# Kernel tuning notes

Hardware: AMD Instinct MI355X
Metric: run time of the kernel (lower is better)

Reference implementation:

```python
import jax, jax.numpy as jnp
import numpy as np

M, K, D_M = 8, 256, 128
N, D = 65536, M * D_M


def setup_inputs() -> dict:
    key = jax.random.key(0)
    kx, kc = jax.random.split(key)
    x = jax.random.normal(kx, (N, D), dtype=jnp.float32)
    codebook = jax.random.normal(kc, (M, K, D_M), dtype=jnp.float32)
    return {"x": x, "codebook": codebook, "temperature": 1}


def _distance(x, codebook):
    # x: (n, d) -> (n, m, d_m); codebook: (m, k, d_m)
    n = x.shape[0]
    m, k, d_m = codebook.shape
    xr = x.reshape(n, m, d_m)
    x2 = jnp.sum(xr * xr, axis=-1, keepdims=True)        # (n, m, 1)
    c2 = jnp.sum(codebook * codebook, axis=-1)            # (m, k)
    inter = jnp.einsum('nmd,mkd->nmk', xr, codebook)      # (n, m, k)
    return x2 + c2 - 2.0 * inter                          # (n, m, k)


def reference(x, codebook, temperature):
    # Soft-PQ (trainable path): soft assignment over codewords per subspace,
    # then reconstruct from the codebook.
    n = x.shape[0]
    m, k, d_m = codebook.shape
    distance = _distance(x, codebook)                     # (n, m, k)
    soft = jax.nn.softmax(-distance / jnp.float32(temperature), axis=-1)
    quantized = jnp.einsum('nmk,mkd->nmd', soft, codebook).reshape(n, m * d_m)
    return quantized
```

## Files before the change

### kernel.cpp

```cpp
#include <hip/hip_runtime.h>

#define LOG2E 1.4426950408889634f

typedef _Float16 half8 __attribute__((ext_vector_type(8)));
typedef float floatx16 __attribute__((ext_vector_type(16)));

__device__ __forceinline__ void g2l16(const void* g, void* l) {
  __builtin_amdgcn_global_load_lds(
      (__attribute__((address_space(1))) void*)(unsigned long long)(g),
      (__attribute__((address_space(3))) void*)(unsigned int)(unsigned long long)(l),
      16, 0, 0);
}

__global__ __launch_bounds__(128, 4) void prep_kernel(
    const float* __restrict__ cb, const int* __restrict__ tptr,
    _Float16* __restrict__ cb16, _Float16* __restrict__ cbT,
    float* __restrict__ c2s) {
  int mk = blockIdx.x;
  int m = mk >> 8, k = mk & 255;
  int d = threadIdx.x;
  float v = cb[(size_t)mk * 128 + d];
  _Float16 h = (_Float16)v;
  cb16[(size_t)mk * 128 + d] = h;
  int kp = ((k & 31) << 3) | (k >> 5);
  cbT[((size_t)m * 128 + d) * 256 + kp] = h;
  float sq = v * v;
#pragma unroll
  for (int o = 0; o < 6; ++o) sq += __shfl_xor(sq, 1 << o, 64);
  __shared__ float part[2];
  if ((threadIdx.x & 63) == 0) part[threadIdx.x >> 6] = sq;
  __syncthreads();
  if (threadIdx.x == 0) {
    float invT = 1.0f / (float)tptr[0];
    c2s[mk] = (part[0] + part[1]) * invT * LOG2E;
  }
}

__global__ __launch_bounds__(256, 2) void pq_kernel(
    const float* __restrict__ x, const int* __restrict__ tptr,
    const _Float16* __restrict__ cb16, const _Float16* __restrict__ cbT,
    const float* __restrict__ c2s, float* __restrict__ out) {
  __shared__ __align__(16) _Float16 smem[37888];
  _Float16* bTile = smem;
  _Float16* pBuf = smem + 4096;

  const int m = blockIdx.x & 7;
  const int tile = blockIdx.x >> 3;
  const int tid = threadIdx.x;
  const int w = tid >> 6;
  const int lane = tid & 63;
  const int n2 = lane & 31;
  const int h = lane >> 5;
  const int rowBase = tile * 128 + w * 32;
  _Float16* pw = pBuf + w * 8448;

  const _Float16* cbm = cb16 + (size_t)m * 256 * 128;
  const _Float16* cbtm = cbT + (size_t)m * 128 * 256;
  const float4* xp = (const float4*)(x + (size_t)(rowBase + n2) * 1024 + m * 128 + h * 8);

  floatx16 acc[8];
#pragma unroll
  for (int t = 0; t < 8; ++t)
#pragma unroll
    for (int i = 0; i < 16; ++i) acc[t][i] = 0.0f;

  for (int kc = 0; kc < 8; ++kc) {
    float4 xa = xp[kc * 4];
    float4 xb = xp[kc * 4 + 1];
    __syncthreads();
#pragma unroll
    for (int i = 0; i < 2; ++i) {
      int c = i * 256 + w * 64 + lane;
      int n = c >> 1, part = c & 1;
      g2l16(cbm + n * 128 + kc * 16 + part * 8, bTile + c * 8);
    }
    __syncthreads();
    float f[8] = {xa.x, xa.y, xa.z, xa.w, xb.x, xb.y, xb.z, xb.w};
    half8 ahi, alo;
#pragma unroll
    for (int j = 0; j < 8; ++j) {
      _Float16 hi = (_Float16)f[j];
      ahi[j] = hi;
      alo[j] = (_Float16)(f[j] - (float)hi);
    }
#pragma unroll
    for (int t = 0; t < 8; ++t) {
      half8 b = *(const half8*)(bTile + (t * 32 + n2) * 16 + h * 8);
      acc[t] = __builtin_amdgcn_mfma_f32_32x32x16_f16(ahi, b, acc[t], 0, 0, 0);
      acc[t] = __builtin_amdgcn_mfma_f32_32x32x16_f16(alo, b, acc[t], 0, 0, 0);
    }
  }

  float invT = 1.0f / (float)tptr[0];
  float kappa = 2.0f * invT * LOG2E;
  float cc[8];
#pragma unroll
  for (int t = 0; t < 8; ++t) cc[t] = c2s[m * 256 + t * 32 + n2];
#pragma unroll
  for (int t = 0; t < 8; ++t)
#pragma unroll
    for (int r = 0; r < 16; ++r) acc[t][r] = acc[t][r] * kappa - cc[t];

#pragma unroll
  for (int r = 0; r < 16; ++r) {
    float mx = acc[0][r];
#pragma unroll
    for (int t = 1; t < 8; ++t) mx = fmaxf(mx, acc[t][r]);
#pragma unroll
    for (int o = 0; o < 5; ++o) mx = fmaxf(mx, __shfl_xor(mx, 1 << o, 64));
    float e[8];
    float s = 0.0f;
#pragma unroll
    for (int t = 0; t < 8; ++t) {
      e[t] = exp2f(acc[t][r] - mx);
      s += e[t];
    }
#pragma unroll
    for (int o = 0; o < 5; ++o) s += __shfl_xor(s, 1 << o, 64);
    float is = 1.0f / s;
    half8 p;
#pragma unroll
    for (int t = 0; t < 8; ++t) p[t] = (_Float16)(e[t] * is);
    int R = (r & 3) + 8 * (r >> 2) + 4 * h;
    *(half8*)(pw + R * 264 + n2 * 8) = p;
  }

  floatx16 acc2[4];
#pragma unroll
  for (int t = 0; t < 4; ++t)
#pragma unroll
    for (int i = 0; i < 16; ++i) acc2[t][i] = 0.0f;

  for (int kc = 0; kc < 8; ++kc) {
    half8 a0 = *(const half8*)(pw + n2 * 264 + kc * 32 + h * 8);
    half8 a1 = *(const half8*)(pw + n2 * 264 + kc * 32 + 16 + h * 8);
    __syncthreads();
#pragma unroll
    for (int i = 0; i < 2; ++i) {
      int c = i * 256 + w * 64 + lane;
      int d = c >> 2, part = c & 3;
      g2l16(cbtm + d * 256 + kc * 32 + part * 8, bTile + c * 8);
    }
    __syncthreads();
#pragma unroll
    for (int dt = 0; dt < 4; ++dt) {
      half8 b0 = *(const half8*)(bTile + (dt * 32 + n2) * 32 + h * 8);
      half8 b1 = *(const half8*)(bTile + (dt * 32 + n2) * 32 + 16 + h * 8);
      acc2[dt] = __builtin_amdgcn_mfma_f32_32x32x16_f16(a0, b0, acc2[dt], 0, 0, 0);
      acc2[dt] = __builtin_amdgcn_mfma_f32_32x32x16_f16(a1, b1, acc2[dt], 0, 0, 0);
    }
  }

  float* op = out + (size_t)rowBase * 1024 + m * 128;
#pragma unroll
  for (int dt = 0; dt < 4; ++dt)
#pragma unroll
    for (int r = 0; r < 16; ++r) {
      int R = (r & 3) + 8 * (r >> 2) + 4 * h;
      op[(size_t)R * 1024 + dt * 32 + n2] = acc2[dt][r];
    }
}

extern "C" void kernel_launch(void* const* d_in, const int* in_sizes, int n_in,
                              void* d_out, int out_size, void* d_ws, size_t ws_size,
                              hipStream_t stream) {
  const float* x = (const float*)d_in[0];
  const float* cb = (const float*)d_in[1];
  const int* tptr = (const int*)d_in[2];

  _Float16* cb16 = (_Float16*)d_ws;
  _Float16* cbT = (_Float16*)((char*)d_ws + 524288);
  float* c2s = (float*)((char*)d_ws + 1048576);
  float* out = (float*)d_out;

  prep_kernel<<<2048, 128, 0, stream>>>(cb, tptr, cb16, cbT, c2s);
  pq_kernel<<<4096, 256, 0, stream>>>(x, tptr, cb16, cbT, c2s, out);
}
```

Before: 528.8 us.

## Transpose MFMA operands, preload whole codebook into swizzled LDS, keep softmax in registers

Swaps the A/B operands of both MFMA stages so each lane holds one row's logits. This makes the softmax max/sum reductions a single cross-half shuffle and lets the probabilities feed the second GEMM straight from registers instead of an LDS round-trip. The full per-subspace codebook (64KB) is loaded into XOR-swizzled LDS in one shot per stage, replacing eight small sync-bracketed tile loads. Output stores become float4 per row, and the transposed-codebook permutation is changed to match the new register layout. It raises register pressure (preloaded x, p0/p1 arrays) and uses 64KB of LDS per block, which may reduce occupancy.

```diff
diff --git a/kernel.cpp b/kernel.cpp
--- a/kernel.cpp
+++ b/kernel.cpp
@@ -22,7 +22,7 @@
   float v = cb[(size_t)mk * 128 + d];
   _Float16 h = (_Float16)v;
   cb16[(size_t)mk * 128 + d] = h;
-  int kp = ((k & 31) << 3) | (k >> 5);
+  int kp = (k & 243) | ((k & 4) << 1) | ((k & 8) >> 1);
   cbT[((size_t)m * 128 + d) * 256 + kp] = h;
   float sq = v * v;
 #pragma unroll
@@ -40,9 +40,8 @@
     const float* __restrict__ x, const int* __restrict__ tptr,
     const _Float16* __restrict__ cb16, const _Float16* __restrict__ cbT,
     const float* __restrict__ c2s, float* __restrict__ out) {
-  __shared__ __align__(16) _Float16 smem[37888];
-  _Float16* bTile = smem;
-  _Float16* pBuf = smem + 4096;
+  __shared__ __align__(16) _Float16 smem[32768];
+  char* sb = (char*)smem;
 
   const int m = blockIdx.x & 7;
   const int tile = blockIdx.x >> 3;
@@ -51,12 +50,27 @@
   const int lane = tid & 63;
   const int n2 = lane & 31;
   const int h = lane >> 5;
-  const int rowBase = tile * 128 + w * 32;
-  _Float16* pw = pBuf + w * 8448;
-
-  const _Float16* cbm = cb16 + (size_t)m * 256 * 128;
-  const _Float16* cbtm = cbT + (size_t)m * 128 * 256;
-  const float4* xp = (const float4*)(x + (size_t)(rowBase + n2) * 1024 + m * 128 + h * 8);
+  const int xrow = tile * 128 + w * 32 + n2;
+
+  const char* cbm  = (const char*)(cb16 + (size_t)m * 256 * 128);
+  const char* cbtm = (const char*)(cbT  + (size_t)m * 128 * 256);
+
+  {
+    const int swz = ((tid >> 4) & 7) << 4;
+#pragma unroll
+    for (int i = 0; i < 16; ++i) {
+      int L = (i * 256 + tid) * 16;
+      g2l16(cbm + (L ^ swz), sb + L);
+    }
+  }
+
+  const float* xp = x + (size_t)xrow * 1024 + m * 128 + h * 8;
+  float4 xa[8], xb[8];
+#pragma unroll
+  for (int kc = 0; kc < 4; ++kc) {
+    xa[kc] = *(const float4*)(xp + kc * 16);
+    xb[kc] = *(const float4*)(xp + kc * 16 + 4);
+  }
 
   floatx16 acc[8];
 #pragma unroll
@@ -64,66 +78,93 @@
 #pragma unroll
     for (int i = 0; i < 16; ++i) acc[t][i] = 0.0f;
 
+  __syncthreads();
+
+  const int rsw = (n2 & 7) << 4;
+
+#pragma unroll
   for (int kc = 0; kc < 8; ++kc) {
-    float4 xa = xp[kc * 4];
-    float4 xb = xp[kc * 4 + 1];
-    __syncthreads();
-#pragma unroll
-    for (int i = 0; i < 2; ++i) {
-      int c = i * 256 + w * 64 + lane;
-      int n = c >> 1, part = c & 1;
-      g2l16(cbm + n * 128 + kc * 16 + part * 8, bTile + c * 8);
-    }
-    __syncthreads();
-    float f[8] = {xa.x, xa.y, xa.z, xa.w, xb.x, xb.y, xb.z, xb.w};
-    half8 ahi, alo;
+    if (kc == 2) {
+#pragma unroll
+      for (int k2 = 4; k2 < 8; ++k2) {
+        xa[k2] = *(const float4*)(xp + k2 * 16);
+        xb[k2] = *(const float4*)(xp + k2 * 16 + 4);
+      }
+    }
+    float f[8] = {xa[kc].x, xa[kc].y, xa[kc].z, xa[kc].w,
+                  xb[kc].x, xb[kc].y, xb[kc].z, xb[kc].w};
+    half8 bhi, blo;
 #pragma unroll
     for (int j = 0; j < 8; ++j) {
       _Float16 hi = (_Float16)f[j];
-      ahi[j] = hi;
-      alo[j] = (_Float16)(f[j] - (float)hi);
+      bhi[j] = hi;
+      blo[j] = (_Float16)(f[j] - (float)hi);
     }
 #pragma unroll
     for (int t = 0; t < 8; ++t) {
-      half8 b = *(const half8*)(bTile + (t * 32 + n2) * 16 + h * 8);
-      acc[t] = __builtin_amdgcn_mfma_f32_32x32x16_f16(ahi, b, acc[t], 0, 0, 0);
-      acc[t] = __builtin_amdgcn_mfma_f32_32x32x16_f16(alo, b, acc[t], 0, 0, 0);
-    }
-  }
-
-  float invT = 1.0f / (float)tptr[0];
-  float kappa = 2.0f * invT * LOG2E;
-  float cc[8];
-#pragma unroll
-  for (int t = 0; t < 8; ++t) cc[t] = c2s[m * 256 + t * 32 + n2];
+      int addr = (((t * 32 + n2) * 256) + kc * 32 + h * 16) ^ rsw;
+      half8 a = *(const half8*)(sb + addr);
+      acc[t] = __builtin_amdgcn_mfma_f32_32x32x16_f16(a, bhi, acc[t], 0, 0, 0);
+      acc[t] = __builtin_amdgcn_mfma_f32_32x32x16_f16(a, blo, acc[t], 0, 0, 0);
+    }
+  }
+
+  __syncthreads();
+
+  {
+    const int swz2 = ((tid >> 5) & 7) << 4;
+#pragma unroll
+    for (int i = 0; i < 16; ++i) {
+      int L = (i * 256 + tid) * 16;
+      g2l16(cbtm + (L ^ swz2), sb + L);
+    }
+  }
+
+  const float invT = 1.0f / (float)tptr[0];
+  const float kappa = 2.0f * invT * LOG2E;
+  const float4* c2p = (const float4*)(c2s + m * 256) + h;
+
+  float mx = -3.0e38f;
+#pragma unroll
+  for (int t = 0; t < 8; ++t) {
+    float4 cq[4];
+#pragma unroll
+    for (int q = 0; q < 4; ++q) cq[q] = c2p[t * 8 + q * 2];
+    float cf[16] = {cq[0].x, cq[0].y, cq[0].z, cq[0].w,
+                    cq[1].x, cq[1].y, cq[1].z, cq[1].w,
+                    cq[2].x, cq[2].y, cq[2].z, cq[2].w,
+                    cq[3].x, cq[3].y, cq[3].z, cq[3].w};
+#pragma unroll
+    for (int r = 0; r < 16; ++r) {
+      float v = acc[t][r] * kappa - cf[r];
+      acc[t][r] = v;
+      mx = fmaxf(mx, v);
+    }
+  }
+  mx = fmaxf(mx, __shfl_xor(mx, 32));
+
+  float s = 0.0f;
 #pragma unroll
   for (int t = 0; t < 8; ++t)
 #pragma unroll
-    for (int r = 0; r < 16; ++r) acc[t][r] = acc[t][r] * kappa - cc[t];
-
-#pragma unroll
-  for (int r = 0; r < 16; ++r) {
-    float mx = acc[0][r];
-#pragma unroll
-    for (int t = 1; t < 8; ++t) mx = fmaxf(mx, acc[t][r]);
-#pragma unroll
-    for (int o = 0; o < 5; ++o) mx = fmaxf(mx, __shfl_xor(mx, 1 << o, 64));
-    float e[8];
-    float s = 0.0f;
-#pragma unroll
-    for (int t = 0; t < 8; ++t) {
-      e[t] = exp2f(acc[t][r] - mx);
-      s += e[t];
-    }
-#pragma unroll
-    for (int o = 0; o < 5; ++o) s += __shfl_xor(s, 1 << o, 64);
-    float is = 1.0f / s;
-    half8 p;
-#pragma unroll
-    for (int t = 0; t < 8; ++t) p[t] = (_Float16)(e[t] * is);
-    int R = (r & 3) + 8 * (r >> 2) + 4 * h;
-    *(half8*)(pw + R * 264 + n2 * 8) = p;
-  }
+    for (int r = 0; r < 16; ++r) {
+      float e = exp2f(acc[t][r] - mx);
+      acc[t][r] = e;
+      s += e;
+    }
+  s += __shfl_xor(s, 32);
+  const float is = 1.0f / s;
+
+  half8 p0[8], p1[8];
+#pragma unroll
+  for (int t = 0; t < 8; ++t) {
+#pragma unroll
+    for (int r = 0; r < 8; ++r) p0[t][r] = (_Float16)(acc[t][r] * is);
+#pragma unroll
+    for (int r = 0; r < 8; ++r) p1[t][r] = (_Float16)(acc[t][8 + r] * is);
+  }
+
+  __syncthreads();
 
   floatx16 acc2[4];
 #pragma unroll
@@ -131,33 +172,25 @@
 #pragma unroll
     for (int i = 0; i < 16; ++i) acc2[t][i] = 0.0f;
 
-  for (int kc = 0; kc < 8; ++kc) {
-    half8 a0 = *(const half8*)(pw + n2 * 264 + kc * 32 + h * 8);
-    half8 a1 = *(const half8*)(pw + n2 * 264 + kc * 32 + 16 + h * 8);
-    __syncthreads();
-#pragma unroll
-    for (int i = 0; i < 2; ++i) {
-      int c = i * 256 + w * 64 + lane;
-      int d = c >> 2, part = c & 3;
-      g2l16(cbtm + d * 256 + kc * 32 + part * 8, bTile + c * 8);
-    }
-    __syncthreads();
+#pragma unroll
+  for (int kc = 0; kc < 16; ++kc) {
+    half8 b = (kc & 1) ? p1[kc >> 1] : p0[kc >> 1];
 #pragma unroll
     for (int dt = 0; dt < 4; ++dt) {
-      half8 b0 = *(const half8*)(bTile + (dt * 32 + n2) * 32 + h * 8);
-      half8 b1 = *(const half8*)(bTile + (dt * 32 + n2) * 32 + 16 + h * 8);
-      acc2[dt] = __builtin_amdgcn_mfma_f32_32x32x16_f16(a0, b0, acc2[dt], 0, 0, 0);
-      acc2[dt] = __builtin_amdgcn_mfma_f32_32x32x16_f16(a1, b1, acc2[dt], 0, 0, 0);
-    }
-  }
-
-  float* op = out + (size_t)rowBase * 1024 + m * 128;
+      int addr = (((dt * 32 + n2) * 512) + kc * 32 + h * 16) ^ rsw;
+      half8 a = *(const half8*)(sb + addr);
+      acc2[dt] = __builtin_amdgcn_mfma_f32_32x32x16_f16(a, b, acc2[dt], 0, 0, 0);
+    }
+  }
+
+  float* op = out + (size_t)xrow * 1024 + m * 128 + h * 4;
 #pragma unroll
   for (int dt = 0; dt < 4; ++dt)
 #pragma unroll
-    for (int r = 0; r < 16; ++r) {
-      int R = (r & 3) + 8 * (r >> 2) + 4 * h;
-      op[(size_t)R * 1024 + dt * 32 + n2] = acc2[dt][r];
+    for (int q = 0; q < 4; ++q) {
+      float4 v = {acc2[dt][q * 4 + 0], acc2[dt][q * 4 + 1],
+                  acc2[dt][q * 4 + 2], acc2[dt][q * 4 + 3]};
+      *(float4*)(op + dt * 32 + q * 8) = v;
     }
 }
 
```

Result: faster. 505.6 us (-4.4%).
